# Optimization experiments

Measured on AMD Instinct MI355X. Metric: run time of the kernel, lower is better.

## Reference

```python
import jax, jax.numpy as jnp
import numpy as np

NUM_STEPS = 20
START_IDX = 1


def setup_inputs() -> dict:
    key = jax.random.key(0)
    ks = jax.random.split(key, 14)
    B, L, D, H, E, K, V = 128, 49, 2048, 2048, 512, 512, 10000
    s = 0.02  # weight init scale to avoid saturating tanh/sigmoid
    return {
        "spatial": jax.random.normal(ks[0], (B, L, D), jnp.float32),
        "global_": jax.random.normal(ks[1], (B, D), jnp.float32),
        "embed": jax.random.normal(ks[2], (V, E), jnp.float32) * s,
        "W_ih": jax.random.normal(ks[3], (4 * H, E + D), jnp.float32) * s,
        "W_hh": jax.random.normal(ks[4], (4 * H, H), jnp.float32) * s,
        "b_ih": jnp.zeros((4 * H,), jnp.float32),
        "b_hh": jnp.zeros((4 * H,), jnp.float32),
        "W_v": jax.random.normal(ks[5], (D, K), jnp.float32) * s,
        "W_g": jax.random.normal(ks[6], (H, K), jnp.float32) * s,
        "w_h": jax.random.normal(ks[7], (K,), jnp.float32) * s,
        "W_p_w": jax.random.normal(ks[8], (V, H), jnp.float32) * s,
        "W_p_b": jnp.zeros((V,), jnp.float32),
        "W_init_h": jax.random.normal(ks[9], (D, H), jnp.float32) * s,
        "W_init_m": jax.random.normal(ks[10], (D, H), jnp.float32) * s,
    }


def reference(spatial, global_, embed, W_ih, W_hh, b_ih, b_hh,
              W_v, W_g, w_h, W_p_w, W_p_b, W_init_h, W_init_m):
    B = spatial.shape[0]
    Hdim = W_hh.shape[1]
    # initialize_state(features.global_)
    h0 = jnp.tanh(global_ @ W_init_h)
    m0 = jnp.tanh(global_ @ W_init_m)
    tok0 = jnp.full((B,), START_IDX, dtype=jnp.int32)
    # precompute attention projection of spatial features: [B, L, K]
    spatial_proj = jnp.einsum('bld,dk->blk', spatial, W_v)

    def step(carry, _):
        h, m, token = carry
        w = embed[token]                                  # [B, E]
        x = jnp.concatenate([w, global_], axis=1)         # [B, E+D]
        gates = x @ W_ih.T + b_ih + h @ W_hh.T + b_hh     # [B, 4H]
        i_g, f_g, g_g, o_g = jnp.split(gates, 4, axis=1)  # torch gate order
        m_new = jax.nn.sigmoid(f_g) * m + jax.nn.sigmoid(i_g) * jnp.tanh(g_g)
        h_new = jax.nn.sigmoid(o_g) * jnp.tanh(m_new)
        # spatial attention: z = w_h^T tanh(W_v V + W_g h)
        z = jnp.tanh(spatial_proj + (h_new @ W_g)[:, None, :]) @ w_h  # [B, L]
        alpha = jax.nn.softmax(z, axis=1)
        c = jnp.einsum('bl,bld->bd', alpha, spatial)      # [B, D]
        logits = (c + h_new) @ W_p_w.T + W_p_b            # [B, V]
        token_new = jnp.argmax(logits, axis=1).astype(jnp.int32)
        return (h_new, m_new, token_new), (logits, token_new)

    _, (logits_seq, tokens) = jax.lax.scan(step, (h0, m0, tok0), None, length=NUM_STEPS)
    # [T, B, V] -> [B, T, V]; [T, B] -> [B, T]
    return jnp.transpose(logits_seq, (1, 0, 2)), tokens.T
```

## Files before the change

kernel.cpp:

```cpp
#include <hip/hip_runtime.h>
#include <math.h>


typedef __attribute__((ext_vector_type(8))) short bf16x8;
typedef __attribute__((ext_vector_type(4))) float f32x4;

#define B_ 128
#define L_ 49
#define D_ 2048
#define H_ 2048
#define E_ 512
#define KA_ 512
#define V_ 10000
#define T_ 20
#define ED_ 2560
#define KT_ 4608
#define KT2_ 2560
#define H4_ 8192
#define VP_ 10112

__device__ __forceinline__ void split1(float x, short* hi, short* lo){
  unsigned u = __float_as_uint(x);
  *hi = (short)(u >> 16);
  float r = x - __uint_as_float(u & 0xffff0000u);
  *lo = (short)(__float_as_uint(r) >> 16);
}
__device__ __forceinline__ void split8(float4 a, float4 b, bf16x8& h, bf16x8& l){
  float xs[8] = {a.x,a.y,a.z,a.w,b.x,b.y,b.z,b.w};
#pragma unroll
  for (int i=0;i<8;++i){
    unsigned u = __float_as_uint(xs[i]);
    h[i] = (short)(u>>16);
    float r = xs[i] - __uint_as_float(u & 0xffff0000u);
    l[i] = (short)(__float_as_uint(r)>>16);
  }
}

#define MFMA16(d,a,b,c) d = __builtin_amdgcn_mfma_f32_16x16x32_bf16(a,b,c,0,0,0)

__device__ __forceinline__ void gl_lds16(const short* g, char* l){
  __builtin_amdgcn_global_load_lds(
      (const __attribute__((address_space(1))) unsigned int*)g,
      (__attribute__((address_space(3))) unsigned int*)l, 16, 0, 0);
}

__global__ __launch_bounds__(256)
void gemm_lds(const short* __restrict__ A1h, const short* __restrict__ A1l, int lda1,
              const short* __restrict__ A2h, const short* __restrict__ A2l, int lda2,
              int ksplit,
              const short* __restrict__ Wh, const short* __restrict__ Wl, int ldw,
              float* __restrict__ Cp, int Mtot, int Np, int k_len)
{
  __shared__ __align__(16) char smem[65536];
  const int tid = threadIdx.x;
  const int wid = tid >> 6, lane = tid & 63;
  const int lr = lane & 15, lg = lane >> 4;
  const int m0 = blockIdx.z * 128;
  const int nblk = blockIdx.x * 128;
  const int kb0 = blockIdx.y * k_len;

  const int li8 = lane >> 3;
  const int kx  = 8 * ((lane & 7) ^ li8);

  f32x4 acc[8][2];
#pragma unroll
  for (int i=0;i<8;++i)
#pragma unroll
    for (int r=0;r<4;++r){ acc[i][0][r]=0.f; acc[i][1][r]=0.f; }

  const int rA = wid*32 + lr, rB = rA + 16;
  const int sw7 = lr & 7;

  for (int kt = 0; kt < k_len; kt += 64) {
    const int kb = kb0 + kt;
    if (wid == 0) {
#pragma unroll
      for (int j = 0; j < 16; ++j)
        gl_lds16(Wh + (long)(nblk + j*8 + li8)*ldw + kb + kx, smem + j*1024);
    } else if (wid == 1) {
#pragma unroll
      for (int j = 0; j < 16; ++j)
        gl_lds16(Wl + (long)(nblk + j*8 + li8)*ldw + kb + kx, smem + 16384 + j*1024);
    } else {
      const short *Ph, *Pl; int ldx, kc;
      if (kb < ksplit) { Ph = A1h; Pl = A1l; ldx = lda1; kc = kb; }
      else             { Ph = A2h; Pl = A2l; ldx = lda2; kc = kb - ksplit; }
      if (wid == 2) {
#pragma unroll
        for (int j = 0; j < 16; ++j)
          gl_lds16(Ph + (long)(m0 + j*8 + li8)*ldx + kc + kx, smem + 32768 + j*1024);
      } else {
#pragma unroll
        for (int j = 0; j < 16; ++j)
          gl_lds16(Pl + (long)(m0 + j*8 + li8)*ldx + kc + kx, smem + 49152 + j*1024);
      }
    }
    asm volatile("s_waitcnt vmcnt(0)");
    __syncthreads();

#pragma unroll
    for (int h = 0; h < 2; ++h) {
      const int c16 = (h<<2) + lg;
      const int swz = (c16 ^ sw7) << 4;
      const bf16x8 whA = *(const bf16x8*)(smem +         rA*128 + swz);
      const bf16x8 wlA = *(const bf16x8*)(smem + 16384 + rA*128 + swz);
      const bf16x8 whB = *(const bf16x8*)(smem +         rB*128 + swz);
      const bf16x8 wlB = *(const bf16x8*)(smem + 16384 + rB*128 + swz);
#pragma unroll
      for (int mt = 0; mt < 8; ++mt) {
        const int aoff = (mt*16 + lr)*128 + swz;
        const bf16x8 ah = *(const bf16x8*)(smem + 32768 + aoff);
        const bf16x8 al = *(const bf16x8*)(smem + 49152 + aoff);
        MFMA16(acc[mt][0], ah, whA, acc[mt][0]);
        MFMA16(acc[mt][1], ah, whB, acc[mt][1]);
        MFMA16(acc[mt][0], ah, wlA, acc[mt][0]);
        MFMA16(acc[mt][1], ah, wlB, acc[mt][1]);
        MFMA16(acc[mt][0], al, whA, acc[mt][0]);
        MFMA16(acc[mt][1], al, whB, acc[mt][1]);
      }
    }
    __syncthreads();
  }

  const long srow = (long)blockIdx.y * Mtot + m0;
#pragma unroll
  for (int mt=0; mt<8; ++mt)
#pragma unroll
    for (int nt=0; nt<2; ++nt){
      const int col = nblk + wid*32 + nt*16 + lr;
#pragma unroll
      for (int r=0; r<4; ++r)
        Cp[(srow + mt*16 + 4*lg + r)*Np + col] = acc[mt][nt][r];
    }
}

__global__ __launch_bounds__(256)
void gemm_db(const short* __restrict__ A1h, const short* __restrict__ A1l, int lda1,
             const short* __restrict__ A2h, const short* __restrict__ A2l, int lda2,
             int ksplit,
             const short* __restrict__ Wh, const short* __restrict__ Wl, int ldw,
             float* __restrict__ Cp, int Mtot, int Np, int k_len)
{
  __shared__ __align__(16) char smem[131072];
  const int tid = threadIdx.x;
  const int wid = tid >> 6, lane = tid & 63;
  const int lr = lane & 15, lg = lane >> 4;
  const int m0 = blockIdx.z * 128;
  const int nblk = blockIdx.x * 128;
  const int kb0 = blockIdx.y * k_len;

  const int li8 = lane >> 3;
  const int kx  = 8 * ((lane & 7) ^ li8);

  f32x4 acc[8][2];
#pragma unroll
  for (int i=0;i<8;++i)
#pragma unroll
    for (int r=0;r<4;++r){ acc[i][0][r]=0.f; acc[i][1][r]=0.f; }

  const int rA = wid*32 + lr, rB = rA + 16;
  const int sw7 = lr & 7;

  auto STAGE = [&](int kb, int buf) {
    char* s = smem + buf*65536;
    if (wid == 0) {
#pragma unroll
      for (int j = 0; j < 16; ++j)
        gl_lds16(Wh + (long)(nblk + j*8 + li8)*ldw + kb + kx, s + j*1024);
    } else if (wid == 1) {
#pragma unroll
      for (int j = 0; j < 16; ++j)
        gl_lds16(Wl + (long)(nblk + j*8 + li8)*ldw + kb + kx, s + 16384 + j*1024);
    } else {
      const short *Ph, *Pl; int ldx, kc;
      if (kb < ksplit) { Ph = A1h; Pl = A1l; ldx = lda1; kc = kb; }
      else             { Ph = A2h; Pl = A2l; ldx = lda2; kc = kb - ksplit; }
      if (wid == 2) {
#pragma unroll
        for (int j = 0; j < 16; ++j)
          gl_lds16(Ph + (long)(m0 + j*8 + li8)*ldx + kc + kx, s + 32768 + j*1024);
      } else {
#pragma unroll
        for (int j = 0; j < 16; ++j)
          gl_lds16(Pl + (long)(m0 + j*8 + li8)*ldx + kc + kx, s + 49152 + j*1024);
      }
    }
  };

  auto COMPUTE = [&](int buf) {
    char* s = smem + buf*65536;
#pragma unroll
    for (int h = 0; h < 2; ++h) {
      const int c16 = (h<<2) + lg;
      const int swz = (c16 ^ sw7) << 4;
      const bf16x8 whA = *(const bf16x8*)(s +         rA*128 + swz);
      const bf16x8 wlA = *(const bf16x8*)(s + 16384 + rA*128 + swz);
      const bf16x8 whB = *(const bf16x8*)(s +         rB*128 + swz);
      const bf16x8 wlB = *(const bf16x8*)(s + 16384 + rB*128 + swz);
#pragma unroll
      for (int mt = 0; mt < 8; ++mt) {
        const int aoff = (mt*16 + lr)*128 + swz;
        const bf16x8 ah = *(const bf16x8*)(s + 32768 + aoff);
        const bf16x8 al = *(const bf16x8*)(s + 49152 + aoff);
        MFMA16(acc[mt][0], ah, whA, acc[mt][0]);
        MFMA16(acc[mt][1], ah, whB, acc[mt][1]);
        MFMA16(acc[mt][0], ah, wlA, acc[mt][0]);
        MFMA16(acc[mt][1], ah, wlB, acc[mt][1]);
        MFMA16(acc[mt][0], al, whA, acc[mt][0]);
        MFMA16(acc[mt][1], al, whB, acc[mt][1]);
      }
    }
  };

  STAGE(kb0, 0);
  asm volatile("s_waitcnt vmcnt(0)");
  __syncthreads();
  int cur = 0;
  for (int kt = 64; kt < k_len; kt += 64) {
    STAGE(kb0 + kt, cur ^ 1);
    COMPUTE(cur);
    asm volatile("s_waitcnt vmcnt(0)");
    __syncthreads();
    cur ^= 1;
  }
  COMPUTE(cur);

  const long srow = (long)blockIdx.y * Mtot + m0;
#pragma unroll
  for (int mt=0; mt<8; ++mt)
#pragma unroll
    for (int nt=0; nt<2; ++nt){
      const int col = nblk + wid*32 + nt*16 + lr;
#pragma unroll
      for (int r=0; r<4; ++r)
        Cp[(srow + mt*16 + 4*lg + r)*Np + col] = acc[mt][nt][r];
    }
}

template<bool AF32>
__global__ __launch_bounds__(256)
void gemm_mfma(const void* Ahv, const void* Alv, int lda,
               const float* __restrict__ W1, int ldw1,
               const float* __restrict__ W2, int ldw2, int ksplit,
               float* __restrict__ Cp, int Mtot, int Np, int Nvalid, int k_len)
{
  const int tid = threadIdx.x;
  const int wid = tid >> 6, lane = tid & 63;
  const int lr = lane & 15, lg = lane >> 4;
  const int m0 = blockIdx.z * 128;
  const int nw = blockIdx.x * 128 + wid * 32;
  const int kb = blockIdx.y * k_len;

  int rowA = nw + lr;       if (rowA >= Nvalid) rowA = Nvalid - 1;
  int rowB = nw + 16 + lr;  if (rowB >= Nvalid) rowB = Nvalid - 1;

  f32x4 acc[8][2];
#pragma unroll
  for (int i=0;i<8;++i)
#pragma unroll
    for (int r=0;r<4;++r){ acc[i][0][r]=0.f; acc[i][1][r]=0.f; }

  for (int kk = 0; kk < k_len; kk += 32) {
    const int kg = kb + kk;
    const float *pA, *pB;
    if (W2 && kg >= ksplit) {
      pA = W2 + (long)rowA*ldw2 + (kg - ksplit) + 8*lg;
      pB = W2 + (long)rowB*ldw2 + (kg - ksplit) + 8*lg;
    } else {
      pA = W1 + (long)rowA*ldw1 + kg + 8*lg;
      pB = W1 + (long)rowB*ldw1 + kg + 8*lg;
    }
    bf16x8 whA, wlA, whB, wlB;
    split8(*(const float4*)pA, *(const float4*)(pA+4), whA, wlA);
    split8(*(const float4*)pB, *(const float4*)(pB+4), whB, wlB);

    bf16x8 ah[8], al[8];
    if constexpr (AF32) {
      const float* Af = (const float*)Ahv;
#pragma unroll
      for (int mt=0; mt<8; ++mt){
        const float* ap = Af + (long)(m0 + mt*16 + lr)*lda + kg + 8*lg;
        split8(*(const float4*)ap, *(const float4*)(ap+4), ah[mt], al[mt]);
      }
    } else {
      const short* Ah = (const short*)Ahv;
      const short* Al = (const short*)Alv;
#pragma unroll
      for (int mt=0; mt<8; ++mt){
        const long off = (long)(m0 + mt*16 + lr)*lda + kg + 8*lg;
        ah[mt] = *(const bf16x8*)(Ah + off);
        al[mt] = *(const bf16x8*)(Al + off);
      }
    }
#pragma unroll
    for (int mt=0; mt<8; ++mt){
      MFMA16(acc[mt][0], ah[mt], whA, acc[mt][0]);
      MFMA16(acc[mt][1], ah[mt], whB, acc[mt][1]);
      MFMA16(acc[mt][0], ah[mt], wlA, acc[mt][0]);
      MFMA16(acc[mt][1], ah[mt], wlB, acc[mt][1]);
      MFMA16(acc[mt][0], al[mt], whA, acc[mt][0]);
      MFMA16(acc[mt][1], al[mt], whB, acc[mt][1]);
    }
  }

  const long srow = (long)blockIdx.y * Mtot + m0;
#pragma unroll
  for (int mt=0; mt<8; ++mt)
#pragma unroll
    for (int nt=0; nt<2; ++nt){
      const int col = nw + nt*16 + lr;
#pragma unroll
      for (int r=0; r<4; ++r)
        Cp[(srow + mt*16 + 4*lg + r)*Np + col] = acc[mt][nt][r];
    }
}

__global__ __launch_bounds__(256)
void split_nt_k(const float* __restrict__ W, int src_ld, int Nv, int kcount,
                short* __restrict__ Wh, short* __restrict__ Wl, int ldo, int ko)
{
  const int n = blockIdx.y;
  const int k = blockIdx.x * 1024 + threadIdx.x * 4;
  if (k >= kcount) return;
  short4 hv, lv;
  if (n < Nv) {
    const float4 v = *(const float4*)&W[(long)n*src_ld + k];
    split1(v.x, &hv.x, &lv.x); split1(v.y, &hv.y, &lv.y);
    split1(v.z, &hv.z, &lv.z); split1(v.w, &hv.w, &lv.w);
  } else {
    hv.x=hv.y=hv.z=hv.w=0; lv.x=lv.y=lv.z=lv.w=0;
  }
  *(short4*)&Wh[(long)n*ldo + ko + k] = hv;
  *(short4*)&Wl[(long)n*ldo + ko + k] = lv;
}

__global__ __launch_bounds__(256)
void split_t_k(const float* __restrict__ in, int K, int N,
               short* __restrict__ Oh, short* __restrict__ Ol)
{
  __shared__ float t[64][65];
  const int tid = threadIdx.x;
  const int c0 = blockIdx.x * 64, r0 = blockIdx.y * 64;
  const int lx = tid & 63, ly = tid >> 6;
#pragma unroll
  for (int i = 0; i < 16; ++i)
    t[ly + 4*i][lx] = in[(long)(r0 + ly + 4*i) * N + c0 + lx];
  __syncthreads();
#pragma unroll
  for (int i = 0; i < 16; ++i) {
    short hh, ll;
    split1(t[lx][ly + 4*i], &hh, &ll);
    const long o = (long)(c0 + ly + 4*i) * K + r0 + lx;
    Oh[o] = hh; Ol[o] = ll;
  }
}

__global__ __launch_bounds__(256)
void split_plane_k(const float* __restrict__ in, long n,
                   short* __restrict__ oh, short* __restrict__ ol)
{
  const long i = ((long)blockIdx.x * 256 + threadIdx.x) * 4;
  if (i >= n) return;
  const float4 v = *(const float4*)&in[i];
  short4 hv, lv;
  split1(v.x, &hv.x, &lv.x); split1(v.y, &hv.y, &lv.y);
  split1(v.z, &hv.z, &lv.z); split1(v.w, &hv.w, &lv.w);
  *(short4*)&oh[i] = hv;
  *(short4*)&ol[i] = lv;
}

__global__ __launch_bounds__(256)
void transpose_f32(const float* __restrict__ in, int R, int C, float* __restrict__ out)
{
  __shared__ float t[64][65];
  const int tid = threadIdx.x;
  const int c0 = blockIdx.x * 64, r0 = blockIdx.y * 64;
  const int lx = tid & 63, ly = tid >> 6;
#pragma unroll
  for (int i = 0; i < 16; ++i)
    t[ly + 4*i][lx] = in[(long)(r0 + ly + 4*i) * C + c0 + lx];
  __syncthreads();
#pragma unroll
  for (int i = 0; i < 16; ++i)
    out[(long)(c0 + ly + 4*i) * R + r0 + lx] = t[lx][ly + 4*i];
}

template<int S>
__global__ void reduce_sp_k(const float4* __restrict__ p, float4* __restrict__ sp)
{
  const long i = (long)blockIdx.x * 256 + threadIdx.x;
  const long s = 802816;
  float4 r; r.x = 0.f; r.y = 0.f; r.z = 0.f; r.w = 0.f;
#pragma unroll
  for (int sl = 0; sl < S; ++sl) {
    const float4 v = p[i + sl*s];
    r.x += v.x; r.y += v.y; r.z += v.z; r.w += v.w;
  }
  sp[i] = r;
}

template<int S>
__global__ __launch_bounds__(256)
void gred_k(const float* __restrict__ prt, const float* __restrict__ b_ih,
            const float* __restrict__ b_hh, float* __restrict__ gconst)
{
  const int idx = blockIdx.x * 256 + threadIdx.x;
  const int n = idx & (H4_ - 1);
  float s = b_ih[n] + b_hh[n];
#pragma unroll
  for (int sl = 0; sl < S; ++sl) s += prt[(long)sl * (B_*H4_) + idx];
  gconst[idx] = s;
}

__global__ void init_tok_k(int* tok) {
  if (threadIdx.x < B_) tok[threadIdx.x] = 1;
}

__global__ __launch_bounds__(256)
void reduce_tanh_k(const float* __restrict__ gp, int S, float* __restrict__ out,
                   short* __restrict__ ohi, short* __restrict__ olo)
{
  const int idx = blockIdx.x * 256 + threadIdx.x;
  float s = 0.f;
  for (int sl = 0; sl < S; ++sl) s += gp[(long)sl * (B_*H_) + idx];
  s = tanhf(s);
  out[idx] = s;
  if (ohi) split1(s, &ohi[idx], &olo[idx]);
}

__global__ void gather_emb_k(const float* __restrict__ embed, const int* __restrict__ tok,
                             short* __restrict__ xe_hi, short* __restrict__ xe_lo)
{
  const int b = blockIdx.x, tid = threadIdx.x;
  const int tk = tok[b];
  const float* e = embed + (long)tk * E_;
  for (int i = tid; i < E_; i += 256) split1(e[i], &xe_hi[(long)b*E_ + i], &xe_lo[(long)b*E_ + i]);
}

__global__ void gather_xh_k(const float* __restrict__ embed, const float* __restrict__ global_,
                            const short* __restrict__ h_hi, const short* __restrict__ h_lo,
                            const int* __restrict__ tok,
                            short* __restrict__ xh_hi, short* __restrict__ xh_lo)
{
  const int b = blockIdx.x, tid = threadIdx.x;
  const int tk = tok[b];
  short* rh = xh_hi + (long)b * KT_;
  short* rl = xh_lo + (long)b * KT_;
  const float* e = embed + (long)tk * E_;
  for (int i = tid; i < E_; i += 256) split1(e[i], &rh[i], &rl[i]);
  for (int i = tid; i < D_; i += 256) split1(global_[(long)b * D_ + i], &rh[E_ + i], &rl[E_ + i]);
  for (int i = tid; i < H_; i += 256) { rh[ED_ + i] = h_hi[(long)b * H_ + i]; rl[ED_ + i] = h_lo[(long)b * H_ + i]; }
}

template<int S>
__global__ __launch_bounds__(256)
void lstm_reduce_k(const float* __restrict__ gp, const float* __restrict__ gconst,
                   const float* __restrict__ b1, const float* __restrict__ b2,
                   float* __restrict__ h, float* __restrict__ m,
                   short* __restrict__ h_hi, short* __restrict__ h_lo)
{
  const int idx = blockIdx.x * 256 + threadIdx.x;
  const int b = idx >> 11, n = idx & (H_ - 1);
  float g[4];
#pragma unroll
  for (int j = 0; j < 4; ++j) {
    float s = gconst ? gconst[(long)b * H4_ + j*H_ + n] : (b1[j*H_ + n] + b2[j*H_ + n]);
#pragma unroll
    for (int sl = 0; sl < S; ++sl) s += gp[((long)sl * B_ + b) * H4_ + j*H_ + n];
    g[j] = s;
  }
  const float si = 1.f / (1.f + expf(-g[0]));
  const float sf = 1.f / (1.f + expf(-g[1]));
  const float gg = tanhf(g[2]);
  const float so = 1.f / (1.f + expf(-g[3]));
  const float mn = sf * m[idx] + si * gg;
  const float hn = so * tanhf(mn);
  m[idx] = mn; h[idx] = hn;
  split1(hn, &h_hi[idx], &h_lo[idx]);
}

__global__ __launch_bounds__(256)
void hgz_k(const float* __restrict__ hgp, const float* __restrict__ sp,
           const float* __restrict__ w_h, float* __restrict__ z)
{
  const int b = blockIdx.x, tid = threadIdx.x;
  const int wv = tid >> 6, lane = tid & 63;
  __shared__ float hgs[KA_];
  __shared__ float whs[KA_];
  for (int i = tid; i < KA_; i += 256) {
    float s = 0.f;
#pragma unroll
    for (int sl = 0; sl < 32; ++sl) s += hgp[((long)sl * B_ + b) * KA_ + i];
    hgs[i] = s; whs[i] = w_h[i];
  }
  __syncthreads();
  const int k0 = lane * 8;
  for (int l = wv; l < L_; l += 4) {
    const float4* spv = (const float4*)(sp + ((long)b * L_ + l) * KA_ + k0);
    const float4 s1 = spv[0], s2 = spv[1];
    float s = whs[k0]   * tanhf(s1.x + hgs[k0])
            + whs[k0+1] * tanhf(s1.y + hgs[k0+1])
            + whs[k0+2] * tanhf(s1.z + hgs[k0+2])
            + whs[k0+3] * tanhf(s1.w + hgs[k0+3])
            + whs[k0+4] * tanhf(s2.x + hgs[k0+4])
            + whs[k0+5] * tanhf(s2.y + hgs[k0+5])
            + whs[k0+6] * tanhf(s2.z + hgs[k0+6])
            + whs[k0+7] * tanhf(s2.w + hgs[k0+7]);
#pragma unroll
    for (int off = 32; off > 0; off >>= 1) s += __shfl_down(s, off);
    if (lane == 0) z[b * L_ + l] = s;
  }
}

__global__ __launch_bounds__(256)
void cfull_k(const float* __restrict__ z, const float* __restrict__ spatial,
             const float* __restrict__ h,
             short* __restrict__ a_hi, short* __restrict__ a_lo)
{
  const int b = blockIdx.x, dh = blockIdx.y, tid = threadIdx.x;
  const int lane = tid & 63;
  __shared__ float alph[L_];
  if (tid < 64) {
    float v = (lane < L_) ? z[b * L_ + lane] : -INFINITY;
    float mx = v;
#pragma unroll
    for (int off = 32; off > 0; off >>= 1) mx = fmaxf(mx, __shfl_xor(mx, off));
    float e = (lane < L_) ? expf(v - mx) : 0.f;
    float sum = e;
#pragma unroll
    for (int off = 32; off > 0; off >>= 1) sum += __shfl_xor(sum, off);
    if (lane < L_) alph[lane] = e / sum;
  }
  __syncthreads();
  const int d4 = dh * 256 + tid;
  const float4* sp4 = (const float4*)spatial;
  float4 acc = ((const float4*)h)[(long)b * 512 + d4];
#pragma unroll 7
  for (int l = 0; l < L_; ++l) {
    const float w = alph[l];
    const float4 v = sp4[((long)b * L_ + l) * 512 + d4];
    acc.x = fmaf(w, v.x, acc.x); acc.y = fmaf(w, v.y, acc.y);
    acc.z = fmaf(w, v.z, acc.z); acc.w = fmaf(w, v.w, acc.w);
  }
  short4 hv, lv;
  split1(acc.x, &hv.x, &lv.x); split1(acc.y, &hv.y, &lv.y);
  split1(acc.z, &hv.z, &lv.z); split1(acc.w, &hv.w, &lv.w);
  *(short4*)&a_hi[(long)b * D_ + d4*4] = hv;
  *(short4*)&a_lo[(long)b * D_ + d4*4] = lv;
}

template<int SHG>
__global__ __launch_bounds__(256)
void attn_k(const float* __restrict__ sp_proj, const float* __restrict__ hgp,
            const float* __restrict__ w_h, const float* __restrict__ spatial,
            const float* __restrict__ h,
            short* __restrict__ a_hi, short* __restrict__ a_lo)
{
  const int b = blockIdx.x, half = blockIdx.y, tid = threadIdx.x;
  const int lane = tid & 63, wv = tid >> 6;
  __shared__ float hgs[KA_];
  __shared__ float whs[KA_];
  __shared__ float zs[L_];
  __shared__ float alph[L_];
  for (int i = tid; i < KA_; i += 256) {
    float s = 0.f;
#pragma unroll
    for (int sl = 0; sl < SHG; ++sl) s += hgp[((long)sl * B_ + b) * KA_ + i];
    hgs[i] = s; whs[i] = w_h[i];
  }
  __syncthreads();
  for (int l = wv; l < L_; l += 4) {
    const float* sp = sp_proj + ((long)b * L_ + l) * KA_;
    float s = 0.f;
    for (int k = lane; k < KA_; k += 64) s += whs[k] * tanhf(sp[k] + hgs[k]);
#pragma unroll
    for (int off = 32; off > 0; off >>= 1) s += __shfl_down(s, off);
    if (lane == 0) zs[l] = s;
  }
  __syncthreads();
  if (wv == 0) {
    float v = (lane < L_) ? zs[lane] : -INFINITY;
    float mx = v;
#pragma unroll
    for (int off = 32; off > 0; off >>= 1) mx = fmaxf(mx, __shfl_xor(mx, off));
    float e = (lane < L_) ? expf(v - mx) : 0.f;
    float sum = e;
#pragma unroll
    for (int off = 32; off > 0; off >>= 1) sum += __shfl_xor(sum, off);
    if (lane < L_) alph[lane] = e / sum;
  }
  __syncthreads();
  const int d4 = half * 256 + tid;
  const float4* h4 = (const float4*)h;
  const float4* sp4 = (const float4*)spatial;
  float4 acc = h4[(long)b * 512 + d4];
#pragma unroll 7
  for (int l = 0; l < L_; ++l) {
    const float w = alph[l];
    const float4 v = sp4[((long)b * L_ + l) * 512 + d4];
    acc.x = fmaf(w, v.x, acc.x); acc.y = fmaf(w, v.y, acc.y);
    acc.z = fmaf(w, v.z, acc.z); acc.w = fmaf(w, v.w, acc.w);
  }
  short4 hv, lv;
  split1(acc.x, &hv.x, &lv.x); split1(acc.y, &hv.y, &lv.y);
  split1(acc.z, &hv.z, &lv.z); split1(acc.w, &hv.w, &lv.w);
  *(short4*)&a_hi[(long)b * D_ + d4*4] = hv;
  *(short4*)&a_lo[(long)b * D_ + d4*4] = lv;
}

template<int S>
__global__ __launch_bounds__(256)
void logits_part_k(const float* __restrict__ lp, const float* __restrict__ bias,
                   float* __restrict__ outL, float* __restrict__ cval,
                   int* __restrict__ cidx)
{
  const int b = blockIdx.x, s8 = blockIdx.y, tid = threadIdx.x;
  const int j0 = s8 * 1264;
  float bv = -INFINITY; int bi = 0x7fffffff;
  for (int j = j0 + tid; j < j0 + 1264; j += 256) {
    if (j < V_) {
      float v = bias[j];
#pragma unroll
      for (int sl = 0; sl < S; ++sl) v += lp[((long)sl * B_ + b) * VP_ + j];
      outL[(long)b * (T_*V_) + j] = v;
      if (v > bv) { bv = v; bi = j; }
    }
  }
  __shared__ float sv[256];
  __shared__ int   si[256];
  sv[tid] = bv; si[tid] = bi;
  __syncthreads();
  for (int s = 128; s > 0; s >>= 1) {
    if (tid < s) {
      const float ov = sv[tid + s]; const int oi = si[tid + s];
      if (ov > sv[tid] || (ov == sv[tid] && oi < si[tid])) { sv[tid] = ov; si[tid] = oi; }
    }
    __syncthreads();
  }
  if (tid == 0) { cval[b*8 + s8] = sv[0]; cidx[b*8 + s8] = si[0]; }
}

__global__ __launch_bounds__(256)
void argmax_fin_k(const float* __restrict__ cval, const int* __restrict__ cidx,
                  int* __restrict__ tok, float* __restrict__ tokout,
                  const float* __restrict__ embed,
                  short* __restrict__ xe_hi, short* __restrict__ xe_lo)
{
  const int b = blockIdx.x, tid = threadIdx.x;
  __shared__ int stk;
  if (tid == 0) {
    float bv = cval[b*8]; int bi = cidx[b*8];
#pragma unroll
    for (int s = 1; s < 8; ++s) {
      const float v = cval[b*8 + s]; const int i = cidx[b*8 + s];
      if (v > bv || (v == bv && i < bi)) { bv = v; bi = i; }
    }
    tok[b] = bi; tokout[(long)b * T_] = (float)bi; stk = bi;
  }
  __syncthreads();
  const float* e = embed + (long)stk * E_;
  for (int i = tid; i < E_; i += 256)
    split1(e[i], &xe_hi[(long)b*E_ + i], &xe_lo[(long)b*E_ + i]);
}

template<int S>
__global__ __launch_bounds__(256)
void logits_argmax_k(const float* __restrict__ lp, const float* __restrict__ bias,
                     float* __restrict__ outL, int* __restrict__ tok,
                     float* __restrict__ tokout)
{
  const int b = blockIdx.x, tid = threadIdx.x;
  float bv = -INFINITY; int bi = 0x7fffffff;
  for (int j = tid; j < V_; j += 256) {
    float v = bias[j];
#pragma unroll
    for (int sl = 0; sl < S; ++sl) v += lp[((long)sl * B_ + b) * VP_ + j];
    outL[(long)b * (T_*V_) + j] = v;
    if (v > bv) { bv = v; bi = j; }
  }
  __shared__ float sv[256];
  __shared__ int   si[256];
  sv[tid] = bv; si[tid] = bi;
  __syncthreads();
  for (int s = 128; s > 0; s >>= 1) {
    if (tid < s) {
      const float ov = sv[tid + s]; const int oi = si[tid + s];
      if (ov > sv[tid] || (ov == sv[tid] && oi < si[tid])) { sv[tid] = ov; si[tid] = oi; }
    }
    __syncthreads();
  }
  if (tid == 0) { tok[b] = si[0]; tokout[(long)b * T_] = (float)si[0]; }
}

extern "C" void kernel_launch(void* const* d_in, const int* in_sizes, int n_in,
                              void* d_out, int out_size, void* d_ws, size_t ws_size,
                              hipStream_t stream)
{
  const float* spatial  = (const float*)d_in[0];
  const float* global_  = (const float*)d_in[1];
  const float* embed    = (const float*)d_in[2];
  const float* W_ih     = (const float*)d_in[3];
  const float* W_hh     = (const float*)d_in[4];
  const float* b_ih     = (const float*)d_in[5];
  const float* b_hh     = (const float*)d_in[6];
  const float* W_v      = (const float*)d_in[7];
  const float* W_g      = (const float*)d_in[8];
  const float* w_h      = (const float*)d_in[9];
  const float* W_p_w    = (const float*)d_in[10];
  const float* W_p_b    = (const float*)d_in[11];
  const float* W_init_h = (const float*)d_in[12];
  const float* W_init_m = (const float*)d_in[13];
  float* out = (float*)d_out;
  float* tokout = out + (long)B_ * T_ * V_;

  char* base = (char*)d_ws;
  const size_t NEED_PRE = 284983808;
  const size_t NEED_FB  = 62390784;
  if (ws_size < NEED_FB) return;

  if (ws_size >= NEED_PRE) {
    float* sp      = (float*)(base + 0);
    float* h       = (float*)(base + 12845056);
    float* m       = (float*)(base + 13893632);
    short* h_hi    = (short*)(base + 14942208);
    short* h_lo    = (short*)(base + 15466496);
    short* a_hi    = (short*)(base + 15990784);
    short* a_lo    = (short*)(base + 16515072);
    short* xe_hi   = (short*)(base + 17039360);
    short* xe_lo   = (short*)(base + 17170432);
    short* g_hi    = (short*)(base + 18350080);
    short* g_lo    = (short*)(base + 18874368);
    float* gconst  = (float*)(base + 19398656);
    int*   tok     = (int*)  (base + 23592960);
    float* arena   = (float*)(base + 23593472);
    short* Wcat_hi = (short*)(base + 107479552);
    short* Wcat_lo = (short*)(base + 149422592);
    short* Wp_hi   = (short*)(base + 191365632);
    short* Wp_lo   = (short*)(base + 232784384);
    short* WvT_hi  = (short*)(base + 274203136);
    short* WvT_lo  = (short*)(base + 276300288);
    short* WgT_hi  = (short*)(base + 278397440);
    short* WgT_lo  = (short*)(base + 280494592);
    float* zbuf    = (float*)(base + 282853888);
    float* cval    = (float*)(base + 282886656);
    int*   cidx    = (int*)  (base + 282890752);

    init_tok_k<<<1, 128, 0, stream>>>(tok);
    split_plane_k<<<256, 256, 0, stream>>>(global_, (long)B_*D_, g_hi, g_lo);

    split_t_k<<<dim3(KA_/64, D_/64), 256, 0, stream>>>(W_v, D_, KA_, WvT_hi, WvT_lo);
    short* spA_hi = Wp_hi;
    short* spA_lo = (short*)((char*)Wp_hi + 25690112);
    split_plane_k<<<12544, 256, 0, stream>>>(spatial, (long)B_*L_*D_, spA_hi, spA_lo);
    float* sppart = (float*)Wcat_hi;
    gemm_db<<<dim3(4, 2, 49), 256, 0, stream>>>(
        spA_hi, spA_lo, D_, spA_hi, spA_lo, D_, 1<<30,
        WvT_hi, WvT_lo, D_, sppart, B_*L_, KA_, 1024);
    reduce_sp_k<2><<<3136, 256, 0, stream>>>((const float4*)sppart, (float4*)sp);

    short* Wglob_hi = Wp_hi;
    short* Wglob_lo = (short*)((char*)Wp_hi + 33554432);
    split_nt_k<<<dim3(2, H4_), 256, 0, stream>>>(W_ih + 512, ED_, H4_, D_, Wglob_hi, Wglob_lo, D_, 0);
    gemm_db<<<dim3(64, 4, 1), 256, 0, stream>>>(
        g_hi, g_lo, D_, g_hi, g_lo, D_, 1<<30,
        Wglob_hi, Wglob_lo, D_, arena, B_, H4_, 512);
    gred_k<4><<<(B_*H4_)/256, 256, 0, stream>>>(arena, b_ih, b_hh, gconst);

    split_nt_k<<<dim3(1, H4_), 256, 0, stream>>>(W_ih, ED_, H4_, E_, Wcat_hi, Wcat_lo, KT2_, 0);
    split_nt_k<<<dim3(2, H4_), 256, 0, stream>>>(W_hh, H_, H4_, H_, Wcat_hi, Wcat_lo, KT2_, E_);
    split_nt_k<<<dim3(2, VP_), 256, 0, stream>>>(W_p_w, H_, V_, H_, Wp_hi, Wp_lo, H_, 0);
    split_t_k<<<dim3(KA_/64, H_/64), 256, 0, stream>>>(W_g, H_, KA_, WgT_hi, WgT_lo);

    {
      short* WTh = (short*)arena;
      short* WTl = (short*)((char*)arena + 8388608);
      float* prt = (float*)((char*)arena + 16777216);
      split_t_k<<<dim3(H_/64, D_/64), 256, 0, stream>>>(W_init_h, D_, H_, WTh, WTl);
      gemm_lds<<<dim3(16, 16, 1), 256, 0, stream>>>(
          g_hi, g_lo, D_, g_hi, g_lo, D_, 1<<30,
          WTh, WTl, D_, prt, B_, H_, 128);
      reduce_tanh_k<<<(B_*H_)/256, 256, 0, stream>>>(prt, 16, h, h_hi, h_lo);
      split_t_k<<<dim3(H_/64, D_/64), 256, 0, stream>>>(W_init_m, D_, H_, WTh, WTl);
      gemm_lds<<<dim3(16, 16, 1), 256, 0, stream>>>(
          g_hi, g_lo, D_, g_hi, g_lo, D_, 1<<30,
          WTh, WTl, D_, prt, B_, H_, 128);
      reduce_tanh_k<<<(B_*H_)/256, 256, 0, stream>>>(prt, 16, m, nullptr, nullptr);
    }

    gather_emb_k<<<B_, 256, 0, stream>>>(embed, tok, xe_hi, xe_lo);

    for (int t = 0; t < T_; ++t) {
      gemm_lds<<<dim3(64, 8, 1), 256, 0, stream>>>(
          xe_hi, xe_lo, E_, h_hi, h_lo, H_, E_,
          Wcat_hi, Wcat_lo, KT2_, arena, B_, H4_, 320);
      lstm_reduce_k<8><<<(B_*H_)/256, 256, 0, stream>>>(
          arena, gconst, nullptr, nullptr, h, m, h_hi, h_lo);
      gemm_lds<<<dim3(4, 32, 1), 256, 0, stream>>>(
          h_hi, h_lo, H_, h_hi, h_lo, H_, 1<<30,
          WgT_hi, WgT_lo, H_, arena, B_, KA_, 64);
      hgz_k<<<B_, 256, 0, stream>>>(arena, sp, w_h, zbuf);
      cfull_k<<<dim3(B_, 2), 256, 0, stream>>>(zbuf, spatial, h, a_hi, a_lo);
      gemm_lds<<<dim3(79, 8, 1), 256, 0, stream>>>(
          a_hi, a_lo, H_, a_hi, a_lo, H_, 1<<30,
          Wp_hi, Wp_lo, H_, arena, B_, VP_, 256);
      logits_part_k<8><<<dim3(B_, 8), 256, 0, stream>>>(
          arena, W_p_b, out + (long)t * V_, cval, cidx);
      argmax_fin_k<<<B_, 256, 0, stream>>>(
          cval, cidx, tok, tokout + t, embed, xe_hi, xe_lo);
    }
  } else {
    float* sp    = (float*)(base + 0);
    float* WvTf  = (float*)(base + 12845056);
    float* WgTf  = (float*)(base + 17039360);
    float* h     = (float*)(base + 21233664);
    float* m     = (float*)(base + 22282240);
    short* h_hi  = (short*)(base + 24379392);
    short* h_lo  = (short*)(base + 24903680);
    short* a_hi  = (short*)(base + 25427968);
    short* a_lo  = (short*)(base + 25952256);
    short* xh_hi = (short*)(base + 26476544);
    short* xh_lo = (short*)(base + 27656192);
    int*   tok   = (int*)  (base + 28835840);
    float* arena = (float*)(base + 28836352);

    init_tok_k<<<1, 128, 0, stream>>>(tok);
    transpose_f32<<<dim3(KA_/64, D_/64), 256, 0, stream>>>(W_v, D_, KA_, WvTf);
    gemm_mfma<true><<<dim3(4, 1, 49), 256, 0, stream>>>(
        spatial, nullptr, D_, WvTf, D_, nullptr, 0, 1<<30, sp, B_*L_, KA_, KA_, D_);
    transpose_f32<<<dim3(KA_/64, H_/64), 256, 0, stream>>>(W_g, H_, KA_, WgTf);
    {
      float* WT  = arena;
      float* prt = (float*)((char*)arena + 16777216);
      transpose_f32<<<dim3(H_/64, D_/64), 256, 0, stream>>>(W_init_h, D_, H_, WT);
      gemm_mfma<true><<<dim3(16, 4, 1), 256, 0, stream>>>(
          global_, nullptr, D_, WT, D_, nullptr, 0, 1<<30, prt, B_, H_, H_, 512);
      reduce_tanh_k<<<(B_*H_)/256, 256, 0, stream>>>(prt, 4, h, h_hi, h_lo);
      transpose_f32<<<dim3(H_/64, D_/64), 256, 0, stream>>>(W_init_m, D_, H_, WT);
      gemm_mfma<true><<<dim3(16, 4, 1), 256, 0, stream>>>(
          global_, nullptr, D_, WT, D_, nullptr, 0, 1<<30, prt, B_, H_, H_, 512);
      reduce_tanh_k<<<(B_*H_)/256, 256, 0, stream>>>(prt, 4, m, nullptr, nullptr);
    }
    for (int t = 0; t < T_; ++t) {
      gather_xh_k<<<B_, 256, 0, stream>>>(embed, global_, h_hi, h_lo, tok, xh_hi, xh_lo);
      gemm_mfma<false><<<dim3(64, 8, 1), 256, 0, stream>>>(
          xh_hi, xh_lo, KT_, W_ih, ED_, W_hh, H_, ED_, arena, B_, H4_, H4_, 576);
      lstm_reduce_k<8><<<(B_*H_)/256, 256, 0, stream>>>(
          arena, nullptr, b_ih, b_hh, h, m, h_hi, h_lo);
      gemm_mfma<false><<<dim3(4, 16, 1), 256, 0, stream>>>(
          h_hi, h_lo, H_, WgTf, H_, nullptr, 0, 1<<30, arena, B_, KA_, KA_, 128);
      attn_k<16><<<dim3(B_, 2), 256, 0, stream>>>(sp, arena, w_h, spatial, h, a_hi, a_lo);
      gemm_mfma<false><<<dim3(79, 4, 1), 256, 0, stream>>>(
          a_hi, a_lo, H_, W_p_w, H_, nullptr, 0, 1<<30, arena, B_, VP_, V_, 512);
      logits_argmax_k<4><<<B_, 256, 0, stream>>>(
          arena, W_p_b, out + (long)t * V_, tok, tokout + t);
    }
  }
}
```

Measured before the change: 2.660 ms.

## Fuse attention score and context kernels; replace double-buffered GEMM with LDS GEMM

Merges the per-step attention-score kernel and the softmax/context kernel into one launch, so z stays in shared memory and one launch per step is dropped. The score computation now runs twice, once for each of the two D-halves blocks, which duplicates tanh work. It also removes the double-buffered gemm_db kernel and runs the setup GEMMs for the spatial projection and the global gate constant through gemm_lds with a finer K split and matching reduction counts. The finer split trades more partial sums for more parallel blocks.

Measured after the change: 2.593 ms. -2.5%, faster.

```diff
diff --git a/kernel.cpp b/kernel.cpp
--- a/kernel.cpp
+++ b/kernel.cpp
@@ -134,109 +134,6 @@
     }
 }
 
-__global__ __launch_bounds__(256)
-void gemm_db(const short* __restrict__ A1h, const short* __restrict__ A1l, int lda1,
-             const short* __restrict__ A2h, const short* __restrict__ A2l, int lda2,
-             int ksplit,
-             const short* __restrict__ Wh, const short* __restrict__ Wl, int ldw,
-             float* __restrict__ Cp, int Mtot, int Np, int k_len)
-{
-  __shared__ __align__(16) char smem[131072];
-  const int tid = threadIdx.x;
-  const int wid = tid >> 6, lane = tid & 63;
-  const int lr = lane & 15, lg = lane >> 4;
-  const int m0 = blockIdx.z * 128;
-  const int nblk = blockIdx.x * 128;
-  const int kb0 = blockIdx.y * k_len;
-
-  const int li8 = lane >> 3;
-  const int kx  = 8 * ((lane & 7) ^ li8);
-
-  f32x4 acc[8][2];
-#pragma unroll
-  for (int i=0;i<8;++i)
-#pragma unroll
-    for (int r=0;r<4;++r){ acc[i][0][r]=0.f; acc[i][1][r]=0.f; }
-
-  const int rA = wid*32 + lr, rB = rA + 16;
-  const int sw7 = lr & 7;
-
-  auto STAGE = [&](int kb, int buf) {
-    char* s = smem + buf*65536;
-    if (wid == 0) {
-#pragma unroll
-      for (int j = 0; j < 16; ++j)
-        gl_lds16(Wh + (long)(nblk + j*8 + li8)*ldw + kb + kx, s + j*1024);
-    } else if (wid == 1) {
-#pragma unroll
-      for (int j = 0; j < 16; ++j)
-        gl_lds16(Wl + (long)(nblk + j*8 + li8)*ldw + kb + kx, s + 16384 + j*1024);
-    } else {
-      const short *Ph, *Pl; int ldx, kc;
-      if (kb < ksplit) { Ph = A1h; Pl = A1l; ldx = lda1; kc = kb; }
-      else             { Ph = A2h; Pl = A2l; ldx = lda2; kc = kb - ksplit; }
-      if (wid == 2) {
-#pragma unroll
-        for (int j = 0; j < 16; ++j)
-          gl_lds16(Ph + (long)(m0 + j*8 + li8)*ldx + kc + kx, s + 32768 + j*1024);
-      } else {
-#pragma unroll
-        for (int j = 0; j < 16; ++j)
-          gl_lds16(Pl + (long)(m0 + j*8 + li8)*ldx + kc + kx, s + 49152 + j*1024);
-      }
-    }
-  };
-
-  auto COMPUTE = [&](int buf) {
-    char* s = smem + buf*65536;
-#pragma unroll
-    for (int h = 0; h < 2; ++h) {
-      const int c16 = (h<<2) + lg;
-      const int swz = (c16 ^ sw7) << 4;
-      const bf16x8 whA = *(const bf16x8*)(s +         rA*128 + swz);
-      const bf16x8 wlA = *(const bf16x8*)(s + 16384 + rA*128 + swz);
-      const bf16x8 whB = *(const bf16x8*)(s +         rB*128 + swz);
-      const bf16x8 wlB = *(const bf16x8*)(s + 16384 + rB*128 + swz);
-#pragma unroll
-      for (int mt = 0; mt < 8; ++mt) {
-        const int aoff = (mt*16 + lr)*128 + swz;
-        const bf16x8 ah = *(const bf16x8*)(s + 32768 + aoff);
-        const bf16x8 al = *(const bf16x8*)(s + 49152 + aoff);
-        MFMA16(acc[mt][0], ah, whA, acc[mt][0]);
-        MFMA16(acc[mt][1], ah, whB, acc[mt][1]);
-        MFMA16(acc[mt][0], ah, wlA, acc[mt][0]);
-        MFMA16(acc[mt][1], ah, wlB, acc[mt][1]);
-        MFMA16(acc[mt][0], al, whA, acc[mt][0]);
-        MFMA16(acc[mt][1], al, whB, acc[mt][1]);
-      }
-    }
-  };
-
-  STAGE(kb0, 0);
-  asm volatile("s_waitcnt vmcnt(0)");
-  __syncthreads();
-  int cur = 0;
-  for (int kt = 64; kt < k_len; kt += 64) {
-    STAGE(kb0 + kt, cur ^ 1);
-    COMPUTE(cur);
-    asm volatile("s_waitcnt vmcnt(0)");
-    __syncthreads();
-    cur ^= 1;
-  }
-  COMPUTE(cur);
-
-  const long srow = (long)blockIdx.y * Mtot + m0;
-#pragma unroll
-  for (int mt=0; mt<8; ++mt)
-#pragma unroll
-    for (int nt=0; nt<2; ++nt){
-      const int col = nblk + wid*32 + nt*16 + lr;
-#pragma unroll
-      for (int r=0; r<4; ++r)
-        Cp[(srow + mt*16 + 4*lg + r)*Np + col] = acc[mt][nt][r];
-    }
-}
-
 template<bool AF32>
 __global__ __launch_bounds__(256)
 void gemm_mfma(const void* Ahv, const void* Alv, int lda,
@@ -480,13 +377,17 @@
 }
 
 __global__ __launch_bounds__(256)
-void hgz_k(const float* __restrict__ hgp, const float* __restrict__ sp,
-           const float* __restrict__ w_h, float* __restrict__ z)
-{
-  const int b = blockIdx.x, tid = threadIdx.x;
+void attn_one(const float* __restrict__ hgp, const float* __restrict__ sp,
+              const float* __restrict__ w_h, const float* __restrict__ spatial,
+              const float* __restrict__ h,
+              short* __restrict__ a_hi, short* __restrict__ a_lo)
+{
+  const int b = blockIdx.x, dh = blockIdx.y, tid = threadIdx.x;
   const int wv = tid >> 6, lane = tid & 63;
   __shared__ float hgs[KA_];
   __shared__ float whs[KA_];
+  __shared__ float zs[L_];
+  __shared__ float alph[L_];
   for (int i = tid; i < KA_; i += 256) {
     float s = 0.f;
 #pragma unroll
@@ -508,20 +409,11 @@
             + whs[k0+7] * tanhf(s2.w + hgs[k0+7]);
 #pragma unroll
     for (int off = 32; off > 0; off >>= 1) s += __shfl_down(s, off);
-    if (lane == 0) z[b * L_ + l] = s;
-  }
-}
-
-__global__ __launch_bounds__(256)
-void cfull_k(const float* __restrict__ z, const float* __restrict__ spatial,
-             const float* __restrict__ h,
-             short* __restrict__ a_hi, short* __restrict__ a_lo)
-{
-  const int b = blockIdx.x, dh = blockIdx.y, tid = threadIdx.x;
-  const int lane = tid & 63;
-  __shared__ float alph[L_];
-  if (tid < 64) {
-    float v = (lane < L_) ? z[b * L_ + lane] : -INFINITY;
+    if (lane == 0) zs[l] = s;
+  }
+  __syncthreads();
+  if (wv == 0) {
+    float v = (lane < L_) ? zs[lane] : -INFINITY;
     float mx = v;
 #pragma unroll
     for (int off = 32; off > 0; off >>= 1) mx = fmaxf(mx, __shfl_xor(mx, off));
@@ -741,7 +633,6 @@
     short* WvT_lo  = (short*)(base + 276300288);
     short* WgT_hi  = (short*)(base + 278397440);
     short* WgT_lo  = (short*)(base + 280494592);
-    float* zbuf    = (float*)(base + 282853888);
     float* cval    = (float*)(base + 282886656);
     int*   cidx    = (int*)  (base + 282890752);
 
@@ -753,18 +644,18 @@
     short* spA_lo = (short*)((char*)Wp_hi + 25690112);
     split_plane_k<<<12544, 256, 0, stream>>>(spatial, (long)B_*L_*D_, spA_hi, spA_lo);
     float* sppart = (float*)Wcat_hi;
-    gemm_db<<<dim3(4, 2, 49), 256, 0, stream>>>(
+    gemm_lds<<<dim3(4, 4, 49), 256, 0, stream>>>(
         spA_hi, spA_lo, D_, spA_hi, spA_lo, D_, 1<<30,
-        WvT_hi, WvT_lo, D_, sppart, B_*L_, KA_, 1024);
-    reduce_sp_k<2><<<3136, 256, 0, stream>>>((const float4*)sppart, (float4*)sp);
+        WvT_hi, WvT_lo, D_, sppart, B_*L_, KA_, 512);
+    reduce_sp_k<4><<<3136, 256, 0, stream>>>((const float4*)sppart, (float4*)sp);
 
     short* Wglob_hi = Wp_hi;
     short* Wglob_lo = (short*)((char*)Wp_hi + 33554432);
     split_nt_k<<<dim3(2, H4_), 256, 0, stream>>>(W_ih + 512, ED_, H4_, D_, Wglob_hi, Wglob_lo, D_, 0);
-    gemm_db<<<dim3(64, 4, 1), 256, 0, stream>>>(
+    gemm_lds<<<dim3(64, 8, 1), 256, 0, stream>>>(
         g_hi, g_lo, D_, g_hi, g_lo, D_, 1<<30,
-        Wglob_hi, Wglob_lo, D_, arena, B_, H4_, 512);
-    gred_k<4><<<(B_*H4_)/256, 256, 0, stream>>>(arena, b_ih, b_hh, gconst);
+        Wglob_hi, Wglob_lo, D_, arena, B_, H4_, 256);
+    gred_k<8><<<(B_*H4_)/256, 256, 0, stream>>>(arena, b_ih, b_hh, gconst);
 
     split_nt_k<<<dim3(1, H4_), 256, 0, stream>>>(W_ih, ED_, H4_, E_, Wcat_hi, Wcat_lo, KT2_, 0);
     split_nt_k<<<dim3(2, H4_), 256, 0, stream>>>(W_hh, H_, H4_, H_, Wcat_hi, Wcat_lo, KT2_, E_);
@@ -798,8 +689,7 @@
       gemm_lds<<<dim3(4, 32, 1), 256, 0, stream>>>(
           h_hi, h_lo, H_, h_hi, h_lo, H_, 1<<30,
           WgT_hi, WgT_lo, H_, arena, B_, KA_, 64);
-      hgz_k<<<B_, 256, 0, stream>>>(arena, sp, w_h, zbuf);
-      cfull_k<<<dim3(B_, 2), 256, 0, stream>>>(zbuf, spatial, h, a_hi, a_lo);
+      attn_one<<<dim3(B_, 2), 256, 0, stream>>>(arena, sp, w_h, spatial, h, a_hi, a_lo);
       gemm_lds<<<dim3(79, 8, 1), 256, 0, stream>>>(
           a_hi, a_lo, H_, a_hi, a_lo, H_, 1<<30,
           Wp_hi, Wp_lo, H_, arena, B_, VP_, 256);
```
